# Kernel tuning notes

Measured on AMD Instinct MI355X. Metric: run time of the kernel, lower is better.

## Reference

```python
import jax, jax.numpy as jnp
import numpy as np

N, D, L = 8192, 512, 32


def setup_inputs() -> dict:
    key = jax.random.key(0)
    ks = jax.random.split(key, 14)
    def lin(k, fan_out, fan_in):
        s = 1.0 / np.sqrt(fan_in)
        kw, kb = jax.random.split(k)
        W = jax.random.uniform(kw, (fan_out, fan_in), jnp.float32, -s, s)
        b = jax.random.uniform(kb, (fan_out,), jnp.float32, -s, s)
        return W, b
    xs = jax.random.normal(ks[0], (N, D), jnp.float32)
    W1, b1 = lin(ks[1], 64, D)
    W2, b2 = lin(ks[2], 32, 64)
    W3, b3 = lin(ks[3], L, 32)
    D1, d1 = lin(ks[4], 32, L)
    D2, d2 = lin(ks[5], 64, 32)
    D3, d3 = lin(ks[6], D, 64)
    return {"xs": xs, "W1": W1, "b1": b1, "W2": W2, "b2": b2, "W3": W3, "b3": b3,
            "D1": D1, "d1": d1, "D2": D2, "d2": d2, "D3": D3, "d3": d3}


def reference(xs, W1, b1, W2, b2, W3, b3, D1, d1, D2, d2, D3, d3):
    # Nearest-neighbor (excluding self). Squared distances via Gram trick;
    # argmin over squared dists == argmin over norms, and the original's
    # +1e6*eye diagonal penalty == masking the diagonal with +inf.
    sq = jnp.sum(xs * xs, axis=-1)                     # [N]
    d2m = sq[:, None] + sq[None, :] - 2.0 * (xs @ xs.T)  # [N, N]
    d2m = d2m + jnp.where(jnp.eye(xs.shape[0], dtype=bool), jnp.inf, 0.0)
    closest = jnp.argmin(d2m, axis=1)                  # [N]
    x0s = xs[closest]                                  # [N, D]

    def encoder(x):  # batched tiny MLP, linear in jvp
        h = jax.nn.relu(x @ W1.T + b1)
        h = jax.nn.relu(h @ W2.T + b2)
        return h @ W3.T + b3

    # First-order Taylor expansion around the nearest neighbor:
    # z = f(x0) + Jf(x0) @ (x - x0)
    z0, dz = jax.jvp(encoder, (x0s,), (xs - x0s,))
    zs = z0 + dz                                       # [N, L]

    h = jax.nn.relu(zs @ D1.T + d1)
    h = jax.nn.relu(h @ D2.T + d2)
    x_hats = h @ D3.T + d3                             # [N, D]
    return (x_hats, zs)
```

## Files before the change

### kernel.cpp

```cpp
#include <hip/hip_runtime.h>
#include <hip/hip_bf16.h>

#define NROWS 8192
#define DIM 512
#define NSLOT 194
#define KMASK 0xFFFFE000u
#define QSCALE 21.0f
#define QD2 (-2.0f / (QSCALE * QSCALE))

typedef __attribute__((ext_vector_type(8))) short bf16x8;
typedef __attribute__((ext_vector_type(4))) float f32x4;
typedef __attribute__((ext_vector_type(4))) int i32x4;
typedef __attribute__((ext_vector_type(8))) unsigned short u16x8;

__device__ __forceinline__ float bf2f(unsigned short u) {
    return __uint_as_float(((unsigned int)u) << 16);
}
__device__ __forceinline__ unsigned short f2bf(float f) {
    unsigned int b = __float_as_uint(f);
    return (unsigned short)((b + 0x7FFFu + ((b >> 16) & 1u)) >> 16);
}
__device__ __forceinline__ unsigned char f2i8(float x) {
    float s = x * QSCALE;
    s = fminf(fmaxf(s, -127.f), 127.f);
    const int q = __float2int_rn(s);
    return (unsigned char)(q & 0xFF);
}
__device__ __forceinline__ unsigned int fkey(float f) {
    unsigned int b = __float_as_uint(f);
    return (b & 0x80000000u) ? ~b : (b | 0x80000000u);
}
__device__ __forceinline__ float unfkey(unsigned int u) {
    unsigned int b = (u & 0x80000000u) ? (u ^ 0x80000000u) : ~u;
    return __uint_as_float(b);
}
__device__ __forceinline__ unsigned int minu(unsigned int a, unsigned int b) {
    return a < b ? a : b;
}
__device__ __forceinline__ unsigned int maxu(unsigned int a, unsigned int b) {
    return a > b ? a : b;
}
__device__ __forceinline__ unsigned long long min64(unsigned long long a,
                                                    unsigned long long b) {
    return a < b ? a : b;
}
__device__ __forceinline__ float bcastf(float v, int k) {
    return __uint_as_float((unsigned int)__builtin_amdgcn_readlane(__float_as_uint(v), k));
}

__device__ __forceinline__ void split3(const float* v, u16x8& h8, u16x8& m8, u16x8& l8) {
#pragma unroll
    for (int j = 0; j < 8; ++j) {
        const float x = v[j];
        const unsigned short h = f2bf(x);
        const float r1 = x - bf2f(h);
        const unsigned short m = f2bf(r1);
        const float r2 = r1 - bf2f(m);
        h8[j] = h; m8[j] = m; l8[j] = f2bf(r2);
    }
}
__device__ __forceinline__ void split2(const float* v, u16x8& h8, u16x8& l8) {
#pragma unroll
    for (int j = 0; j < 8; ++j) {
        const float x = v[j];
        const unsigned short h = f2bf(x);
        h8[j] = h; l8[j] = f2bf(x - bf2f(h));
    }
}

__global__ __launch_bounds__(256) void k_prep(const float* __restrict__ xs,
                                              unsigned char* __restrict__ x8,
                                              float* __restrict__ sq) {
    const int tid = threadIdx.x;
    const int wave = tid >> 6, lane = tid & 63;
    const int row = blockIdx.x * 4 + wave;
    const float4* xr = (const float4*)(xs + (size_t)row * DIM);
    const float4 a = xr[2 * lane], b = xr[2 * lane + 1];
    float v[8] = {a.x, a.y, a.z, a.w, b.x, b.y, b.z, b.w};
    unsigned long long pk8 = 0ull;
    float s = 0.f;
#pragma unroll
    for (int i = 0; i < 8; ++i) {
        pk8 |= ((unsigned long long)f2i8(v[i])) << (8 * i);
        s = fmaf(v[i], v[i], s);
    }
    *(unsigned long long*)(x8 + (size_t)row * DIM + lane * 8) = pk8;
#pragma unroll
    for (int d = 32; d; d >>= 1) s += __shfl_xor(s, d);
    if (lane == 0) sq[row] = s;
}

__global__ __launch_bounds__(512, 4) void k_nn(const unsigned char* __restrict__ x8,
                                               const float* __restrict__ sq,
                                               unsigned int* __restrict__ rowtab,
                                               const float* __restrict__ xs,
                                               const float* __restrict__ W1,
                                               float* __restrict__ P) {
    __shared__ __align__(16) unsigned char lsm[32768];
    const int tid = threadIdx.x;
    const int wave = tid >> 6, lane = tid & 63, quad = lane >> 4, ln = lane & 15;

    if (blockIdx.x < 128) {
        unsigned short* lAh = (unsigned short*)(lsm);
        unsigned short* lAm = (unsigned short*)(lsm + 4096);
        unsigned short* lAl = (unsigned short*)(lsm + 8192);
        unsigned short* lWh = (unsigned short*)(lsm + 12288);
        unsigned short* lWm = (unsigned short*)(lsm + 16384);
        unsigned short* lWl = (unsigned short*)(lsm + 20480);
        const int i0 = blockIdx.x * 64;
        const int row = tid >> 2, c = tid & 3;
        const int wofs = row * 32 + ((c + (row >> 1)) & 3) * 8;
        f32x4 acc[4];
#pragma unroll
        for (int ns = 0; ns < 4; ++ns) acc[ns] = (f32x4){0.f, 0.f, 0.f, 0.f};
        const int ar = wave * 16 + ln;
        const int aofs = ar * 32 + ((quad + (ar >> 1)) & 3) * 8;
        int bofs[4];
#pragma unroll
        for (int ns = 0; ns < 4; ++ns) {
            const int br = ns * 16 + ln;
            bofs[ns] = br * 32 + ((quad + (br >> 1)) & 3) * 8;
        }
        for (int kt = 0; kt < 16; ++kt) {
            __syncthreads();
            if (tid < 256) {
                {
                    const float* src = xs + (size_t)(i0 + row) * DIM + kt * 32 + c * 8;
                    const float4 f0 = *(const float4*)src, f1 = *(const float4*)(src + 4);
                    float v[8] = {f0.x, f0.y, f0.z, f0.w, f1.x, f1.y, f1.z, f1.w};
                    u16x8 h8, m8, l8;
                    split3(v, h8, m8, l8);
                    *(u16x8*)(lAh + wofs) = h8;
                    *(u16x8*)(lAm + wofs) = m8;
                    *(u16x8*)(lAl + wofs) = l8;
                }
                {
                    const float* src = W1 + (size_t)row * DIM + kt * 32 + c * 8;
                    const float4 f0 = *(const float4*)src, f1 = *(const float4*)(src + 4);
                    float v[8] = {f0.x, f0.y, f0.z, f0.w, f1.x, f1.y, f1.z, f1.w};
                    u16x8 h8, m8, l8;
                    split3(v, h8, m8, l8);
                    *(u16x8*)(lWh + wofs) = h8;
                    *(u16x8*)(lWm + wofs) = m8;
                    *(u16x8*)(lWl + wofs) = l8;
                }
            }
            __syncthreads();
            if (tid < 256) {
                const bf16x8 ah = *(const bf16x8*)(lAh + aofs);
                const bf16x8 am = *(const bf16x8*)(lAm + aofs);
                const bf16x8 al = *(const bf16x8*)(lAl + aofs);
#pragma unroll
                for (int ns = 0; ns < 4; ++ns) {
                    const bf16x8 bh = *(const bf16x8*)(lWh + bofs[ns]);
                    const bf16x8 bm = *(const bf16x8*)(lWm + bofs[ns]);
                    const bf16x8 bl = *(const bf16x8*)(lWl + bofs[ns]);
                    acc[ns] = __builtin_amdgcn_mfma_f32_16x16x32_bf16(ah, bh, acc[ns], 0, 0, 0);
                    acc[ns] = __builtin_amdgcn_mfma_f32_16x16x32_bf16(ah, bm, acc[ns], 0, 0, 0);
                    acc[ns] = __builtin_amdgcn_mfma_f32_16x16x32_bf16(am, bh, acc[ns], 0, 0, 0);
                    acc[ns] = __builtin_amdgcn_mfma_f32_16x16x32_bf16(am, bm, acc[ns], 0, 0, 0);
                    acc[ns] = __builtin_amdgcn_mfma_f32_16x16x32_bf16(ah, bl, acc[ns], 0, 0, 0);
                    acc[ns] = __builtin_amdgcn_mfma_f32_16x16x32_bf16(al, bh, acc[ns], 0, 0, 0);
                }
            }
        }
        if (tid < 256) {
#pragma unroll
            for (int ns = 0; ns < 4; ++ns)
#pragma unroll
                for (int v = 0; v < 4; ++v)
                    P[(size_t)(i0 + wave * 16 + quad * 4 + v) * 64 + ns * 16 + ln] =
                        acc[ns][v];
        }
        return;
    }

    unsigned char* lA = lsm;
    unsigned char* lB = lsm + 16384;
    const int b = blockIdx.x - 128;
    const int xcd = b & 7, w = b >> 3;
    const int s = w >> 3, bil = w & 7;
    const int bi = xcd * 8 + bil;
    const int bj = (bi + s) & 63;
    const int i0 = bi * 128, j0 = bj * 128;
    const int m_off = (wave >> 1) * 32, n_off = (wave & 1) * 64;

    const int rl = lane >> 2;
    const int sp = ((lane & 3) - ((rl >> 1) & 3)) & 3;
    const unsigned char* gpA = x8 + (size_t)(i0 + wave * 16 + rl) * DIM + sp * 16;
    const unsigned char* gpB = x8 + (size_t)(j0 + wave * 16 + rl) * DIM + sp * 16;
    unsigned char* dstA = lA + wave * 1024;
    unsigned char* dstB = lB + wave * 1024;

    int aoff[2], boff[4];
#pragma unroll
    for (int ms = 0; ms < 2; ++ms) {
        const int r = m_off + ms * 16 + ln;
        aoff[ms] = r * 64 + ((quad + ((r >> 1) & 3)) & 3) * 16;
    }
#pragma unroll
    for (int ns = 0; ns < 4; ++ns) {
        const int r = n_off + ns * 16 + ln;
        boff[ns] = r * 64 + ((quad + ((r >> 1) & 3)) & 3) * 16;
    }

    i32x4 acc[2][4];
#pragma unroll
    for (int a = 0; a < 2; ++a)
#pragma unroll
        for (int c = 0; c < 4; ++c) acc[a][c] = (i32x4){0, 0, 0, 0};

    __builtin_amdgcn_global_load_lds(
        (const __attribute__((address_space(1))) void*)gpA,
        (__attribute__((address_space(3))) void*)dstA, 16, 0, 0);
    __builtin_amdgcn_global_load_lds(
        (const __attribute__((address_space(1))) void*)gpB,
        (__attribute__((address_space(3))) void*)dstB, 16, 0, 0);

#pragma unroll
    for (int kt = 0; kt < 8; ++kt) {
        __syncthreads();
        if (kt < 7) {
            const int nxt = ((kt + 1) & 1) * 8192;
            __builtin_amdgcn_global_load_lds(
                (const __attribute__((address_space(1))) void*)(gpA + (kt + 1) * 64),
                (__attribute__((address_space(3))) void*)(dstA + nxt), 16, 0, 0);
            __builtin_amdgcn_global_load_lds(
                (const __attribute__((address_space(1))) void*)(gpB + (kt + 1) * 64),
                (__attribute__((address_space(3))) void*)(dstB + nxt), 16, 0, 0);
        }
        const int cur = (kt & 1) * 8192;
        i32x4 av[2], bv[4];
#pragma unroll
        for (int ms = 0; ms < 2; ++ms)
            av[ms] = *(const i32x4*)(lA + cur + aoff[ms]);
#pragma unroll
        for (int ns = 0; ns < 4; ++ns)
            bv[ns] = *(const i32x4*)(lB + cur + boff[ns]);
#pragma unroll
        for (int ms = 0; ms < 2; ++ms)
#pragma unroll
            for (int ns = 0; ns < 4; ++ns)
                acc[ms][ns] = __builtin_amdgcn_mfma_i32_16x16x64_i8(
                    av[ms], bv[ns], acc[ms][ns], 0, 0, 0);
    }
    __syncthreads();

    const bool diag = (s == 0);
    float sqj[4];
#pragma unroll
    for (int ns = 0; ns < 4; ++ns) sqj[ns] = sq[j0 + n_off + ns * 16 + ln];
    float sqi[2][4];
#pragma unroll
    for (int ms = 0; ms < 2; ++ms)
#pragma unroll
        for (int v = 0; v < 4; ++v)
            sqi[ms][v] = sq[i0 + m_off + ms * 16 + quad * 4 + v];

    unsigned long long* rowbuf = (unsigned long long*)(void*)lsm + (size_t)wave * 512;

    unsigned int c1[4], c2[4];
#pragma unroll
    for (int ns = 0; ns < 4; ++ns) { c1[ns] = 0xFFFFFFFFu; c2[ns] = 0xFFFFFFFFu; }

#pragma unroll
    for (int ms = 0; ms < 2; ++ms)
#pragma unroll
        for (int v = 0; v < 4; ++v) {
            const int gi = i0 + m_off + ms * 16 + quad * 4 + v;
            const float si = sqi[ms][v];
            unsigned int rp[4];
#pragma unroll
            for (int ns = 0; ns < 4; ++ns) {
                const int gj = j0 + n_off + ns * 16 + ln;
                float d2 = fmaf((float)acc[ms][ns][v], QD2, si + sqj[ns]);
                if (diag && gj == gi) d2 = __builtin_inff();
                const unsigned int ub = (__float_as_uint(d2) | 0x80000000u) & KMASK;
                rp[ns] = ub | (unsigned int)gj;
                const unsigned int cp = ub | (unsigned int)gi;
                c2[ns] = minu(c2[ns], maxu(c1[ns], cp));
                c1[ns] = minu(c1[ns], cp);
            }
            const unsigned int lo1 = minu(rp[0], rp[1]), hi1 = maxu(rp[0], rp[1]);
            const unsigned int lo2 = minu(rp[2], rp[3]), hi2 = maxu(rp[2], rp[3]);
            const unsigned int p1 = minu(lo1, lo2);
            const unsigned int p2 = minu(maxu(lo1, lo2), minu(hi1, hi2));
            const int rloc = ms * 16 + quad * 4 + v;
            rowbuf[rloc * 16 + ln] = (((unsigned long long)p1) << 32) | p2;
        }
    asm volatile("s_waitcnt lgkmcnt(0)" ::: "memory");

    {
        const int rr = lane & 31, hf = lane >> 5;
        unsigned int p1 = 0xFFFFFFFFu, p2 = 0xFFFFFFFFu;
#pragma unroll
        for (int k = 0; k < 8; ++k) {
            const int pos = hf * 8 + (k ^ (rr & 7));
            const unsigned long long pw = rowbuf[rr * 16 + pos];
            const unsigned int a1 = (unsigned int)(pw >> 32), a2 = (unsigned int)pw;
            p2 = minu(minu(p2, a2), maxu(p1, a1));
            p1 = minu(p1, a1);
        }
        const unsigned long long mine = (((unsigned long long)p1) << 32) | p2;
        const unsigned long long oth = __shfl_xor(mine, 32);
        {
            const unsigned int a1 = (unsigned int)(oth >> 32), a2 = (unsigned int)oth;
            p2 = minu(minu(p2, a2), maxu(p1, a1));
            p1 = minu(p1, a1);
        }
        if (lane < 32) {
            const int gi = i0 + m_off + rr;
            const size_t base = ((size_t)gi * NSLOT + (s * 2 + (wave & 1))) * 2;
            rowtab[base] = p1;
            rowtab[base + 1] = p2;
        }
    }

    if (s > 0) {
#pragma unroll
        for (int ns = 0; ns < 4; ++ns) {
            unsigned int q1 = c1[ns], q2 = c2[ns];
#pragma unroll
            for (int d = 16; d <= 32; d <<= 1) {
                const unsigned long long pr = (((unsigned long long)q1) << 32) | q2;
                const unsigned long long o = __shfl_xor(pr, d);
                const unsigned int a1 = (unsigned int)(o >> 32), a2 = (unsigned int)o;
                q2 = minu(minu(q2, a2), maxu(q1, a1));
                q1 = minu(q1, a1);
            }
            if (lane < 16) {
                const int gj = j0 + n_off + ns * 16 + ln;
                const size_t base =
                    ((size_t)gj * NSLOT + (66 + (s - 1) * 4 + (wave >> 1))) * 2;
                rowtab[base] = q1;
                rowtab[base + 1] = q2;
            }
        }
    }
}

__global__ __launch_bounds__(512, 6) void k_refine_mid(
    const unsigned int* __restrict__ rowtab, const float* __restrict__ xs,
    const float* __restrict__ sq, const float* __restrict__ P,
    const float* __restrict__ b1, const float* __restrict__ W2,
    const float* __restrict__ b2, const float* __restrict__ W3,
    const float* __restrict__ b3, const float* __restrict__ D1,
    const float* __restrict__ d1, const float* __restrict__ D2,
    const float* __restrict__ d2, float* __restrict__ out_zs,
    float* __restrict__ G2) {
    __shared__ float W2T[64 * 33], W3T[32 * 33], D1T[32 * 33], D2T[32 * 65];
    __shared__ float b2f[32], b3f[32], d1f[32], d2f[64];
    __shared__ unsigned int clist[4][64];
    __shared__ int ccnt[4];
    __shared__ unsigned int rowbest[4];
    __shared__ unsigned int nnr_s[4];
    __shared__ float pbuf[4][64 * 8];
    const int tid = threadIdx.x;
    const int wave = tid >> 6, lane = tid & 63;
    const int r = wave & 3, half = wave >> 2;
    const int row = blockIdx.x * 4 + r;
    for (int t = tid; t < 2048; t += 512) { int o = t >> 6, k = t & 63; W2T[k * 33 + o] = W2[t]; }
    for (int t = tid; t < 1024; t += 512) { int o = t >> 5, k = t & 31; W3T[k * 33 + o] = W3[t]; }
    for (int t = tid; t < 1024; t += 512) { int o = t >> 5, k = t & 31; D1T[k * 33 + o] = D1[t]; }
    for (int t = tid; t < 2048; t += 512) { int o = t >> 5, k = t & 31; D2T[k * 65 + o] = D2[t]; }
    if (tid < 32) b2f[tid] = b2[tid];
    else if (tid < 64) b3f[tid - 32] = b3[tid - 32];
    else if (tid < 96) d1f[tid - 64] = d1[tid - 64];
    else if (tid < 160) d2f[tid - 96] = d2[tid - 96];
    if (tid < 4) { ccnt[tid] = 0; rowbest[tid] = 0xFFFFFFFFu; }
    __syncthreads();

    unsigned int vals[4];
    int nv = 0;
    unsigned int best = 0xFFFFFFFFu;
    for (int i = half * 64 + lane; i < NSLOT * 2; i += 128) {
        const unsigned int v = rowtab[(size_t)row * NSLOT * 2 + i];
        vals[nv++] = v;
        best = minu(best, v);
    }
#pragma unroll
    for (int d = 1; d < 64; d <<= 1) best = minu(best, __shfl_xor(best, d));
    if (lane == 0) atomicMin(&rowbest[r], best);
    __syncthreads();
    best = rowbest[r];

    const float dmin = unfkey(best & KMASK);
    const unsigned int tkey = fkey(dmin + 5.0f);
    for (int k = 0; k < nv; ++k)
        if ((vals[k] & KMASK) < tkey) {
            const int p = atomicAdd(&ccnt[r], 1);
            if (p < 64) clist[r][p] = vals[k] & 8191u;
        }
    __syncthreads();
    int cnt = ccnt[r];
    cnt = cnt > 64 ? 64 : cnt;

    const float4* xi = (const float4*)(xs + (size_t)row * DIM);
    const float4 x0 = xi[2 * lane], x1 = xi[2 * lane + 1];
    const float sqi = sq[row];
    const int g8 = lane >> 3;
    float4 cy0 = {0.f, 0.f, 0.f, 0.f}, cy1 = {0.f, 0.f, 0.f, 0.f};
    if (half < cnt) {
        const float4* xj = (const float4*)(xs + (size_t)clist[r][half] * DIM);
        cy0 = xj[2 * lane];
        cy1 = xj[2 * lane + 1];
    }
    for (int c = half; c < cnt; c += 2) {
        float4 ny0 = {0.f, 0.f, 0.f, 0.f}, ny1 = {0.f, 0.f, 0.f, 0.f};
        const int cn = c + 2;
        if (cn < cnt) {
            const float4* xj = (const float4*)(xs + (size_t)clist[r][cn] * DIM);
            ny0 = xj[2 * lane];
            ny1 = xj[2 * lane + 1];
        }
        float dot = 0.f;
        dot = fmaf(x0.x, cy0.x, dot); dot = fmaf(x0.y, cy0.y, dot);
        dot = fmaf(x0.z, cy0.z, dot); dot = fmaf(x0.w, cy0.w, dot);
        dot = fmaf(x1.x, cy1.x, dot); dot = fmaf(x1.y, cy1.y, dot);
        dot = fmaf(x1.z, cy1.z, dot); dot = fmaf(x1.w, cy1.w, dot);
        dot += __shfl_xor(dot, 1);
        dot += __shfl_xor(dot, 2);
        dot += __shfl_xor(dot, 4);
        if ((lane & 7) == 0) pbuf[r][c * 8 + g8] = dot;
        cy0 = ny0;
        cy1 = ny1;
    }
    __syncthreads();

    if (half == 0) {
        unsigned long long key = ~0ull;
        if (lane < cnt) {
            const unsigned int j = clist[r][lane];
            float dot = 0.f;
#pragma unroll
            for (int k = 0; k < 8; ++k)
                dot += pbuf[r][lane * 8 + ((k + lane + (lane >> 3)) & 7)];
            const float d2v = sqi + sq[j] - 2.f * dot;
            key = (((unsigned long long)fkey(d2v)) << 32) | j;
        }
#pragma unroll
        for (int d = 1; d < 64; d <<= 1) key = min64(key, __shfl_xor(key, d));
        if (lane == 0) nnr_s[r] = (unsigned int)(key & 0xFFFFFFFFull) & 8191u;
    }
    __syncthreads();
    if (half == 1) return;
    const unsigned int nnr = nnr_s[r];

    const int o32 = lane & 31;
    const float b1v = b1[lane];
    const float pr = P[(size_t)row * 64 + lane];
    const float p0 = P[(size_t)nnr * 64 + lane];
    const float a1 = p0 + b1v;
    const float u1 = pr - p0;
    const float h1 = fmaxf(a1, 0.f);
    const float th1 = (a1 > 0.f) ? u1 : 0.f;
    float a2a = b2f[o32], a2b = 0.f, u2a = 0.f, u2b = 0.f;
#pragma unroll
    for (int k = 0; k < 64; k += 2) {
        const float ha = bcastf(h1, k), hb = bcastf(h1, k + 1);
        const float ta = bcastf(th1, k), tb = bcastf(th1, k + 1);
        const float wa = W2T[k * 33 + o32], wb = W2T[(k + 1) * 33 + o32];
        a2a = fmaf(ha, wa, a2a);
        a2b = fmaf(hb, wb, a2b);
        u2a = fmaf(ta, wa, u2a);
        u2b = fmaf(tb, wb, u2b);
    }
    const float a2 = a2a + a2b;
    const float u2 = u2a + u2b;
    const float sv = fmaxf(a2, 0.f) + ((a2 > 0.f) ? u2 : 0.f);
    float za = b3f[o32], zb = 0.f;
#pragma unroll
    for (int k = 0; k < 32; k += 2) {
        za = fmaf(bcastf(sv, k), W3T[k * 33 + o32], za);
        zb = fmaf(bcastf(sv, k + 1), W3T[(k + 1) * 33 + o32], zb);
    }
    const float z = za + zb;
    if (lane < 32) out_zs[(size_t)row * 32 + lane] = z;
    float g1a = d1f[o32], g1b = 0.f;
#pragma unroll
    for (int k = 0; k < 32; k += 2) {
        g1a = fmaf(bcastf(z, k), D1T[k * 33 + o32], g1a);
        g1b = fmaf(bcastf(z, k + 1), D1T[(k + 1) * 33 + o32], g1b);
    }
    const float g1 = fmaxf(g1a + g1b, 0.f);
    float g2a = d2f[lane], g2b = 0.f;
#pragma unroll
    for (int k = 0; k < 32; k += 2) {
        g2a = fmaf(bcastf(g1, k), D2T[k * 65 + lane], g2a);
        g2b = fmaf(bcastf(g1, k + 1), D2T[(k + 1) * 65 + lane], g2b);
    }
    const float g2 = fmaxf(g2a + g2b, 0.f);
    G2[(size_t)row * 64 + lane] = g2;
}

__global__ __launch_bounds__(512) void k_dec(const float* __restrict__ G2,
                                             const float* __restrict__ D3,
                                             const float* __restrict__ d3,
                                             float* __restrict__ xhat) {
    __shared__ __align__(16) unsigned short lGh[128 * 64], lGl[128 * 64];
    __shared__ __align__(16) unsigned short lDh[128 * 64], lDl[128 * 64];
    const int tid = threadIdx.x, wave = tid >> 6, lane = tid & 63, quad = lane >> 4,
              ln = lane & 15;
    const int i0 = blockIdx.x * 128, nbase = blockIdx.y * 128;
    const int m_off = (wave & 1) * 64, n_off = (wave >> 1) * 32;
#pragma unroll
    for (int r = 0; r < 2; ++r) {
        const int g = r * 512 + tid;
        const int row = g >> 3, cIdx = g & 7, half = cIdx >> 2, cc = cIdx & 3;
        const int wofs = row * 64 + half * 32 + ((cc + (row >> 1)) & 3) * 8;
        {
            const float* src = G2 + (size_t)(i0 + row) * 64 + cIdx * 8;
            const float4 f0 = *(const float4*)src, f1 = *(const float4*)(src + 4);
            float v[8] = {f0.x, f0.y, f0.z, f0.w, f1.x, f1.y, f1.z, f1.w};
            u16x8 h8, l8;
            split2(v, h8, l8);
            *(u16x8*)(lGh + wofs) = h8;
            *(u16x8*)(lGl + wofs) = l8;
        }
        {
            const float* src = D3 + (size_t)(nbase + row) * 64 + cIdx * 8;
            const float4 f0 = *(const float4*)src, f1 = *(const float4*)(src + 4);
            float v[8] = {f0.x, f0.y, f0.z, f0.w, f1.x, f1.y, f1.z, f1.w};
            u16x8 h8, l8;
            split2(v, h8, l8);
            *(u16x8*)(lDh + wofs) = h8;
            *(u16x8*)(lDl + wofs) = l8;
        }
    }
    __syncthreads();
    f32x4 acc[4][2];
#pragma unroll
    for (int a = 0; a < 4; ++a)
#pragma unroll
        for (int c = 0; c < 2; ++c) acc[a][c] = (f32x4){0.f, 0.f, 0.f, 0.f};
#pragma unroll
    for (int kk = 0; kk < 2; ++kk) {
        bf16x8 ah[4], al[4], bh[2], bl[2];
#pragma unroll
        for (int ms = 0; ms < 4; ++ms) {
            const int ar = m_off + ms * 16 + ln;
            const int aofs = ar * 64 + kk * 32 + ((quad + (ar >> 1)) & 3) * 8;
            ah[ms] = *(const bf16x8*)(lGh + aofs);
            al[ms] = *(const bf16x8*)(lGl + aofs);
        }
#pragma unroll
        for (int ns = 0; ns < 2; ++ns) {
            const int br = n_off + ns * 16 + ln;
            const int bofs = br * 64 + kk * 32 + ((quad + (br >> 1)) & 3) * 8;
            bh[ns] = *(const bf16x8*)(lDh + bofs);
            bl[ns] = *(const bf16x8*)(lDl + bofs);
        }
#pragma unroll
        for (int ms = 0; ms < 4; ++ms)
#pragma unroll
            for (int ns = 0; ns < 2; ++ns) {
                acc[ms][ns] = __builtin_amdgcn_mfma_f32_16x16x32_bf16(
                    ah[ms], bh[ns], acc[ms][ns], 0, 0, 0);
                acc[ms][ns] = __builtin_amdgcn_mfma_f32_16x16x32_bf16(
                    ah[ms], bl[ns], acc[ms][ns], 0, 0, 0);
                acc[ms][ns] = __builtin_amdgcn_mfma_f32_16x16x32_bf16(
                    al[ms], bh[ns], acc[ms][ns], 0, 0, 0);
            }
    }
    float d3f[2];
#pragma unroll
    for (int ns = 0; ns < 2; ++ns) d3f[ns] = d3[nbase + n_off + ns * 16 + ln];
#pragma unroll
    for (int ms = 0; ms < 4; ++ms)
#pragma unroll
        for (int ns = 0; ns < 2; ++ns)
#pragma unroll
            for (int v = 0; v < 4; ++v) {
                const int m = m_off + ms * 16 + quad * 4 + v;
                const int n = n_off + ns * 16 + ln;
                xhat[(size_t)(i0 + m) * DIM + nbase + n] = acc[ms][ns][v] + d3f[ns];
            }
}

extern "C" void kernel_launch(void* const* d_in, const int* in_sizes, int n_in,
                              void* d_out, int out_size, void* d_ws, size_t ws_size,
                              hipStream_t stream) {
    const float* xs = (const float*)d_in[0];
    const float* W1 = (const float*)d_in[1];
    const float* b1 = (const float*)d_in[2];
    const float* W2 = (const float*)d_in[3];
    const float* b2 = (const float*)d_in[4];
    const float* W3 = (const float*)d_in[5];
    const float* b3 = (const float*)d_in[6];
    const float* D1 = (const float*)d_in[7];
    const float* d1 = (const float*)d_in[8];
    const float* D2 = (const float*)d_in[9];
    const float* d2 = (const float*)d_in[10];
    const float* D3 = (const float*)d_in[11];
    const float* d3 = (const float*)d_in[12];

    char* ws = (char*)d_ws;
    float* sq = (float*)(ws);
    unsigned char* xs_i8 = (unsigned char*)(ws + 131072);
    float* P = (float*)(ws + 8519680);
    float* G2 = (float*)(ws + 10616832);

    float* xhat = (float*)d_out;
    float* zs = (float*)d_out + (size_t)NROWS * DIM;
    unsigned int* rowtab = (unsigned int*)d_out;

    hipLaunchKernelGGL(k_prep, dim3(2048), dim3(256), 0, stream, xs, xs_i8, sq);
    hipLaunchKernelGGL(k_nn, dim3(2240), dim3(512), 0, stream, xs_i8, sq, rowtab, xs,
                       W1, P);
    hipLaunchKernelGGL(k_refine_mid, dim3(2048), dim3(512), 0, stream, rowtab, xs, sq,
                       P, b1, W2, b2, W3, b3, D1, d1, D2, d2, zs, G2);
    hipLaunchKernelGGL(k_dec, dim3(64, 4), dim3(512), 0, stream, G2, D3, d3, xhat);
}
```

Before: 156.4 us.

## Load int8 GEMM operands directly from global memory instead of LDS staging

The int8 Gram-matrix tile loop no longer stages A and B through double-buffered LDS with global_load_lds and per-iteration barriers. Each wave now reads its MFMA operand fragments straight from global memory, relying on L2/L1 caching. This removes the barriers and LDS traffic, but loses the data sharing between waves, so each wave re-fetches rows that other waves in the block also use.

Measured after the change: 223.9 us. 1.43x slower.

```diff
diff --git a/kernel.cpp b/kernel.cpp
--- a/kernel.cpp
+++ b/kernel.cpp
@@ -175,8 +175,6 @@
         return;
     }
 
-    unsigned char* lA = lsm;
-    unsigned char* lB = lsm + 16384;
     const int b = blockIdx.x - 128;
     const int xcd = b & 7, w = b >> 3;
     const int s = w >> 3, bil = w & 7;
@@ -185,24 +183,14 @@
     const int i0 = bi * 128, j0 = bj * 128;
     const int m_off = (wave >> 1) * 32, n_off = (wave & 1) * 64;
 
-    const int rl = lane >> 2;
-    const int sp = ((lane & 3) - ((rl >> 1) & 3)) & 3;
-    const unsigned char* gpA = x8 + (size_t)(i0 + wave * 16 + rl) * DIM + sp * 16;
-    const unsigned char* gpB = x8 + (size_t)(j0 + wave * 16 + rl) * DIM + sp * 16;
-    unsigned char* dstA = lA + wave * 1024;
-    unsigned char* dstB = lB + wave * 1024;
-
-    int aoff[2], boff[4];
-#pragma unroll
-    for (int ms = 0; ms < 2; ++ms) {
-        const int r = m_off + ms * 16 + ln;
-        aoff[ms] = r * 64 + ((quad + ((r >> 1) & 3)) & 3) * 16;
-    }
-#pragma unroll
-    for (int ns = 0; ns < 4; ++ns) {
-        const int r = n_off + ns * 16 + ln;
-        boff[ns] = r * 64 + ((quad + ((r >> 1) & 3)) & 3) * 16;
-    }
+    const unsigned char* gA[2];
+    const unsigned char* gB[4];
+#pragma unroll
+    for (int ms = 0; ms < 2; ++ms)
+        gA[ms] = x8 + (size_t)(i0 + m_off + ms * 16 + ln) * DIM + quad * 16;
+#pragma unroll
+    for (int ns = 0; ns < 4; ++ns)
+        gB[ns] = x8 + (size_t)(j0 + n_off + ns * 16 + ln) * DIM + quad * 16;
 
     i32x4 acc[2][4];
 #pragma unroll
@@ -210,33 +198,15 @@
 #pragma unroll
         for (int c = 0; c < 4; ++c) acc[a][c] = (i32x4){0, 0, 0, 0};
 
-    __builtin_amdgcn_global_load_lds(
-        (const __attribute__((address_space(1))) void*)gpA,
-        (__attribute__((address_space(3))) void*)dstA, 16, 0, 0);
-    __builtin_amdgcn_global_load_lds(
-        (const __attribute__((address_space(1))) void*)gpB,
-        (__attribute__((address_space(3))) void*)dstB, 16, 0, 0);
-
 #pragma unroll
     for (int kt = 0; kt < 8; ++kt) {
-        __syncthreads();
-        if (kt < 7) {
-            const int nxt = ((kt + 1) & 1) * 8192;
-            __builtin_amdgcn_global_load_lds(
-                (const __attribute__((address_space(1))) void*)(gpA + (kt + 1) * 64),
-                (__attribute__((address_space(3))) void*)(dstA + nxt), 16, 0, 0);
-            __builtin_amdgcn_global_load_lds(
-                (const __attribute__((address_space(1))) void*)(gpB + (kt + 1) * 64),
-                (__attribute__((address_space(3))) void*)(dstB + nxt), 16, 0, 0);
-        }
-        const int cur = (kt & 1) * 8192;
         i32x4 av[2], bv[4];
 #pragma unroll
         for (int ms = 0; ms < 2; ++ms)
-            av[ms] = *(const i32x4*)(lA + cur + aoff[ms]);
+            av[ms] = *(const i32x4*)(gA[ms] + kt * 64);
 #pragma unroll
         for (int ns = 0; ns < 4; ++ns)
-            bv[ns] = *(const i32x4*)(lB + cur + boff[ns]);
+            bv[ns] = *(const i32x4*)(gB[ns] + kt * 64);
 #pragma unroll
         for (int ms = 0; ms < 2; ++ms)
 #pragma unroll
@@ -244,7 +214,6 @@
                 acc[ms][ns] = __builtin_amdgcn_mfma_i32_16x16x64_i8(
                     av[ms], bv[ns], acc[ms][ns], 0, 0, 0);
     }
-    __syncthreads();
 
     const bool diag = (s == 0);
     float sqj[4];
```
